# Performance work log

Measured on AMD Instinct MI355X. Metric: run time of the kernel, lower is better.

## Reference

```python
import jax, jax.numpy as jnp
import numpy as np

N_NODES = 50000
N_EDGES = 500000
H_DIM = 128
BN_EPS = 1e-5


def setup_inputs() -> dict:
    key = jax.random.key(0)
    k1, k2, k3, k4 = jax.random.split(key, 4)
    ent_emb = jax.random.normal(k1, (N_NODES, H_DIM), dtype=jnp.float32)
    neigh_w = jax.random.normal(k2, (H_DIM, H_DIM), dtype=jnp.float32) * 0.05
    gamma = jnp.ones((H_DIM,), dtype=jnp.float32)
    beta = jnp.zeros((H_DIM,), dtype=jnp.float32)
    src = jax.random.randint(k3, (N_EDGES,), 0, N_NODES, dtype=jnp.int32)
    dst = jax.random.randint(k4, (N_EDGES,), 0, N_NODES, dtype=jnp.int32)
    return {"ent_emb": ent_emb, "neigh_w": neigh_w, "gamma": gamma,
            "beta": beta, "src": src, "dst": dst}


def reference(ent_emb, neigh_w, gamma, beta, src, dst):
    # u_dot_v: per-edge dot product of src and dst node embeddings -> [E]
    e_src = ent_emb[src]                      # [E, D] gather
    scores = jnp.sum(e_src * ent_emb[dst], axis=-1)  # [E]

    # edge_softmax: softmax over incoming edges of each destination node
    seg_max = jax.ops.segment_max(scores, dst, num_segments=N_NODES)
    seg_max = jnp.where(jnp.isfinite(seg_max), seg_max, 0.0)  # empty nodes
    ex = jnp.exp(scores - seg_max[dst])
    denom = jax.ops.segment_sum(ex, dst, num_segments=N_NODES)
    norm = ex / denom[dst]                    # [E]

    # u_mul_e + sum: weighted scatter-sum of src embeddings into dst nodes
    neigh = jax.ops.segment_sum(e_src * norm[:, None], dst,
                                num_segments=N_NODES)  # [N, D]

    # linear + BatchNorm1d (training mode, batch stats) + tanh
    h = neigh @ neigh_w
    mu = jnp.mean(h, axis=0)
    var = jnp.var(h, axis=0)                  # biased, matches torch BN
    h = (h - mu) * jax.lax.rsqrt(var + BN_EPS) * gamma + beta
    return jnp.tanh(h)
```

## Files before the change

kernel.cpp:

```cpp
#include <hip/hip_runtime.h>
#include <hip/hip_bf16.h>
#include <math.h>

#define N_NODES 50000
#define N_EDGES 500000
#define H_DIM   128
#define BN_EPS  1e-5f
#define GEMM_GRID ((N_NODES + 31) / 32)
#define SCAN_NBLK ((N_NODES + 255) / 256)
#define RED_NBLK  64

typedef __attribute__((ext_vector_type(8))) short short8;
typedef __attribute__((ext_vector_type(4))) float floatx4;

__device__ __forceinline__ ushort f2bf(float x)
{
    unsigned u = __float_as_uint(x);
    unsigned r = (u + 0x7FFFu + ((u >> 16) & 1u)) >> 16;
    return (ushort)r;
}

__global__ __launch_bounds__(256) void cvt_w_kernel(
    const float* __restrict__ W, ushort* __restrict__ wt)
{
    int i = blockIdx.x * 256 + threadIdx.x;
    if (i >= H_DIM * H_DIM) return;
    int k = i >> 7, c = i & 127;
    wt[c * 128 + k] = f2bf(W[i]);
}

__global__ __launch_bounds__(256) void hist_kernel(
    const int* __restrict__ dst, int* __restrict__ deg)
{
    int e = blockIdx.x * blockDim.x + threadIdx.x;
    if (e < N_EDGES) atomicAdd(&deg[dst[e]], 1);
}

__global__ __launch_bounds__(256) void scan_partial_kernel(
    const int* __restrict__ deg, int* __restrict__ blocksum)
{
    __shared__ int red[256];
    int t = threadIdx.x;
    int i = blockIdx.x * 256 + t;
    red[t] = (i < N_NODES) ? deg[i] : 0;
    __syncthreads();
    #pragma unroll
    for (int off = 128; off; off >>= 1) {
        if (t < off) red[t] += red[t + off];
        __syncthreads();
    }
    if (t == 0) blocksum[blockIdx.x] = red[0];
}

__global__ __launch_bounds__(256) void scan_final_kernel(
    const int* __restrict__ deg, const int* __restrict__ blocksum,
    int* __restrict__ rowptr, int* __restrict__ cursor)
{
    __shared__ int bs[256];
    __shared__ int s[256];
    int t = threadIdx.x;

    bs[t] = (t < SCAN_NBLK) ? blocksum[t] : 0;
    __syncthreads();
    for (int off = 1; off < 256; off <<= 1) {
        int v = (t >= off) ? bs[t - off] : 0;
        __syncthreads();
        bs[t] += v;
        __syncthreads();
    }
    int blockoff = (blockIdx.x == 0) ? 0 : bs[blockIdx.x - 1];

    int i = blockIdx.x * 256 + t;
    int v = (i < N_NODES) ? deg[i] : 0;
    s[t] = v;
    __syncthreads();
    for (int off = 1; off < 256; off <<= 1) {
        int u = (t >= off) ? s[t - off] : 0;
        __syncthreads();
        s[t] += u;
        __syncthreads();
    }
    int excl = s[t] - v + blockoff;
    if (i < N_NODES) {
        rowptr[i] = excl;
        cursor[i] = excl;
        if (i == N_NODES - 1) rowptr[N_NODES] = excl + v;
    }
}

__global__ __launch_bounds__(256) void csr_scatter_kernel(
    const int* __restrict__ src, const int* __restrict__ dst,
    int* __restrict__ cursor, int* __restrict__ csr_src)
{
    int e = blockIdx.x * blockDim.x + threadIdx.x;
    if (e >= N_EDGES) return;
    int pos = atomicAdd(&cursor[dst[e]], 1);
    csr_src[pos] = src[e];
}

__global__ __launch_bounds__(256) void node_aggregate_kernel(
    const float* __restrict__ emb,
    const int* __restrict__ rowptr,
    const int* __restrict__ csr_src,
    float* __restrict__ neigh)
{
    int node = blockIdx.x * 8 + (threadIdx.x >> 5);
    int lane = threadIdx.x & 31;
    if (node >= N_NODES) return;

    int beg = rowptr[node];
    int end = rowptr[node + 1];

    const float4 b = *((const float4*)(emb + (size_t)node * H_DIM) + lane);

    float m = -INFINITY;
    float denom = 0.f;
    float4 acc = {0.f, 0.f, 0.f, 0.f};

    int e = beg;

    for (; e + 8 <= end; e += 8) {
        float4 a[8];
        float  p[8];
        #pragma unroll
        for (int u = 0; u < 8; ++u) {
            int s = csr_src[e + u];
            a[u] = *((const float4*)(emb + (size_t)s * H_DIM) + lane);
        }
        #pragma unroll
        for (int u = 0; u < 8; ++u)
            p[u] = a[u].x * b.x + a[u].y * b.y + a[u].z * b.z + a[u].w * b.w;
        #pragma unroll
        for (int off = 16; off; off >>= 1) {
            #pragma unroll
            for (int u = 0; u < 8; ++u)
                p[u] += __shfl_xor(p[u], off);
        }
        float mn = m;
        #pragma unroll
        for (int u = 0; u < 8; ++u) mn = fmaxf(mn, p[u]);
        float corr = __expf(m - mn);
        float w[8];
        #pragma unroll
        for (int u = 0; u < 8; ++u) w[u] = __expf(p[u] - mn);
        float ws = 0.f;
        #pragma unroll
        for (int u = 0; u < 8; ++u) ws += w[u];
        denom = denom * corr + ws;
        float sx = 0.f, sy = 0.f, sz = 0.f, sw = 0.f;
        #pragma unroll
        for (int u = 0; u < 8; ++u) {
            sx += a[u].x * w[u];
            sy += a[u].y * w[u];
            sz += a[u].z * w[u];
            sw += a[u].w * w[u];
        }
        acc.x = acc.x * corr + sx;
        acc.y = acc.y * corr + sy;
        acc.z = acc.z * corr + sz;
        acc.w = acc.w * corr + sw;
        m = mn;
    }

    if (e + 4 <= end) {
        float4 a[4];
        float  p[4];
        #pragma unroll
        for (int u = 0; u < 4; ++u) {
            int s = csr_src[e + u];
            a[u] = *((const float4*)(emb + (size_t)s * H_DIM) + lane);
        }
        #pragma unroll
        for (int u = 0; u < 4; ++u)
            p[u] = a[u].x * b.x + a[u].y * b.y + a[u].z * b.z + a[u].w * b.w;
        #pragma unroll
        for (int off = 16; off; off >>= 1) {
            #pragma unroll
            for (int u = 0; u < 4; ++u)
                p[u] += __shfl_xor(p[u], off);
        }
        float mn = fmaxf(fmaxf(fmaxf(p[0], p[1]), fmaxf(p[2], p[3])), m);
        float corr = __expf(m - mn);
        float w[4];
        #pragma unroll
        for (int u = 0; u < 4; ++u) w[u] = __expf(p[u] - mn);
        denom = denom * corr + w[0] + w[1] + w[2] + w[3];
        acc.x = acc.x * corr + a[0].x*w[0] + a[1].x*w[1] + a[2].x*w[2] + a[3].x*w[3];
        acc.y = acc.y * corr + a[0].y*w[0] + a[1].y*w[1] + a[2].y*w[2] + a[3].y*w[3];
        acc.z = acc.z * corr + a[0].z*w[0] + a[1].z*w[1] + a[2].z*w[2] + a[3].z*w[3];
        acc.w = acc.w * corr + a[0].w*w[0] + a[1].w*w[1] + a[2].w*w[2] + a[3].w*w[3];
        m = mn;
        e += 4;
    }

    for (; e < end; ++e) {
        int s = csr_src[e];
        float4 a = *((const float4*)(emb + (size_t)s * H_DIM) + lane);
        float p = a.x * b.x + a.y * b.y + a.z * b.z + a.w * b.w;
        #pragma unroll
        for (int off = 16; off; off >>= 1)
            p += __shfl_xor(p, off);
        float mn   = fmaxf(m, p);
        float corr = __expf(m - mn);
        float w    = __expf(p - mn);
        denom = denom * corr + w;
        acc.x = acc.x * corr + a.x * w;
        acc.y = acc.y * corr + a.y * w;
        acc.z = acc.z * corr + a.z * w;
        acc.w = acc.w * corr + a.w * w;
        m = mn;
    }

    float inv = (end > beg) ? (1.0f / denom) : 0.f;
    float4 o = {acc.x * inv, acc.y * inv, acc.z * inv, acc.w * inv};
    *((float4*)(neigh + (size_t)node * H_DIM) + lane) = o;
}

__global__ __launch_bounds__(256) void gemm_stats_kernel(
    const float* __restrict__ neigh,
    const ushort* __restrict__ wt,
    float* __restrict__ h,
    float* __restrict__ partial)
{
    __shared__ ushort A_s[32 * 128];
    __shared__ ushort W_s[128 * 128];
    __shared__ float  red_s[128 * 9];
    __shared__ float  red_q[128 * 9];

    int t  = threadIdx.x;
    int r0 = blockIdx.x * 32;

    for (int g = t; g < 32 * 16; g += 256) {
        int r = g >> 4, gc = g & 15;
        int gr = r0 + r;
        float4 x0 = {0.f,0.f,0.f,0.f}, x1 = {0.f,0.f,0.f,0.f};
        if (gr < N_NODES) {
            const float4* p = (const float4*)(neigh + (size_t)gr * H_DIM + gc * 8);
            x0 = p[0]; x1 = p[1];
        }
        ushort v[8] = {f2bf(x0.x), f2bf(x0.y), f2bf(x0.z), f2bf(x0.w),
                       f2bf(x1.x), f2bf(x1.y), f2bf(x1.z), f2bf(x1.w)};
        int idx = r * 128 + ((gc * 8) ^ ((r & 7) << 3));
        *(short8*)&A_s[idx] = *(short8*)v;
    }
    for (int g = t; g < 128 * 16; g += 256) {
        int c = g >> 4, gk = g & 15;
        short8 v = *(const short8*)(wt + (size_t)c * 128 + gk * 8);
        int idx = c * 128 + ((gk * 8) ^ ((c & 7) << 3));
        *(short8*)&W_s[idx] = v;
    }
    __syncthreads();

    int w    = t >> 6;
    int lane = t & 63;
    int rbase = (w >> 1) * 16;
    int c0    = (w & 1) * 64;
    int l15   = lane & 15;
    int kgrp  = lane >> 4;
    int arow  = rbase + l15;
    int k0l   = kgrp * 8;

    floatx4 acc[4] = {{0.f,0.f,0.f,0.f},{0.f,0.f,0.f,0.f},
                      {0.f,0.f,0.f,0.f},{0.f,0.f,0.f,0.f}};

    #pragma unroll
    for (int ks = 0; ks < 4; ++ks) {
        int k0 = ks * 32 + k0l;
        short8 af = *(const short8*)&A_s[arow * 128 + (k0 ^ ((arow & 7) << 3))];
        #pragma unroll
        for (int ct = 0; ct < 4; ++ct) {
            int col = c0 + ct * 16 + l15;
            short8 bf = *(const short8*)&W_s[col * 128 + (k0 ^ ((col & 7) << 3))];
            acc[ct] = __builtin_amdgcn_mfma_f32_16x16x32_bf16(af, bf, acc[ct], 0, 0, 0);
        }
    }

    int contrib = (w >> 1) * 4 + kgrp;
    #pragma unroll
    for (int ct = 0; ct < 4; ++ct) {
        int col = c0 + ct * 16 + l15;
        float ps = 0.f, pq = 0.f;
        #pragma unroll
        for (int reg = 0; reg < 4; ++reg) {
            float v = acc[ct][reg];
            int gr = r0 + rbase + kgrp * 4 + reg;
            if (gr < N_NODES) h[(size_t)gr * H_DIM + col] = v;
            ps += v;
            pq += v * v;
        }
        red_s[col * 9 + contrib] = ps;
        red_q[col * 9 + contrib] = pq;
    }
    __syncthreads();

    float s = 0.f;
    if (t < 128) {
        #pragma unroll
        for (int q = 0; q < 8; ++q) s += red_s[t * 9 + q];
    } else {
        #pragma unroll
        for (int q = 0; q < 8; ++q) s += red_q[(t - 128) * 9 + q];
    }
    partial[(size_t)blockIdx.x * 256 + t] = s;
}

__global__ __launch_bounds__(256) void reduce_partials_kernel(
    const float* __restrict__ partial, float* __restrict__ partial2)
{
    int t = threadIdx.x;
    int g = blockIdx.x;
    float s = 0.f;
    for (int b = g; b < GEMM_GRID; b += RED_NBLK)
        s += partial[(size_t)b * 256 + t];
    partial2[(size_t)g * 256 + t] = s;
}

__global__ __launch_bounds__(1024) void bn_stats_kernel(
    const float* __restrict__ partial2,
    const float* __restrict__ gamma,
    const float* __restrict__ beta,
    float* __restrict__ scale,
    float* __restrict__ shift)
{
    __shared__ float tot[4][256];
    __shared__ float tot2[256];
    int v = threadIdx.x & 255;
    int q = threadIdx.x >> 8;
    float s = 0.f;
    for (int b = q; b < RED_NBLK; b += 4)
        s += partial2[(size_t)b * 256 + v];
    tot[q][v] = s;
    __syncthreads();
    if (threadIdx.x < 256)
        tot2[v] = tot[0][v] + tot[1][v] + tot[2][v] + tot[3][v];
    __syncthreads();
    if (threadIdx.x < 128) {
        int c = threadIdx.x;
        float cs = tot2[c];
        float cq = tot2[c + 128];
        const float invN = 1.0f / (float)N_NODES;
        float mu  = cs * invN;
        float var = cq * invN - mu * mu;
        float sc  = gamma[c] * rsqrtf(var + BN_EPS);
        scale[c] = sc;
        shift[c] = beta[c] - mu * sc;
    }
}

__global__ __launch_bounds__(256) void bn_tanh_kernel(
    float* __restrict__ h,
    const float* __restrict__ scale,
    const float* __restrict__ shift)
{
    size_t i = (size_t)blockIdx.x * blockDim.x + threadIdx.x;
    size_t idx4 = i * 4;
    if (idx4 >= (size_t)N_NODES * H_DIM) return;
    int c = (int)(idx4 & (H_DIM - 1));
    float4 v = *(float4*)(h + idx4);
    v.x = tanhf(v.x * scale[c + 0] + shift[c + 0]);
    v.y = tanhf(v.y * scale[c + 1] + shift[c + 1]);
    v.z = tanhf(v.z * scale[c + 2] + shift[c + 2]);
    v.w = tanhf(v.w * scale[c + 3] + shift[c + 3]);
    *(float4*)(h + idx4) = v;
}

extern "C" void kernel_launch(void* const* d_in, const int* in_sizes, int n_in,
                              void* d_out, int out_size, void* d_ws, size_t ws_size,
                              hipStream_t stream)
{
    const float* ent_emb = (const float*)d_in[0];
    const float* neigh_w = (const float*)d_in[1];
    const float* gamma   = (const float*)d_in[2];
    const float* beta    = (const float*)d_in[3];
    const int*   src     = (const int*)d_in[4];
    const int*   dst     = (const int*)d_in[5];
    float* out = (float*)d_out;

    float*  neigh    = (float*)d_ws;
    int*    deg      = (int*)(neigh + (size_t)N_NODES * H_DIM);
    int*    rowptr   = deg + N_NODES;
    int*    cursor   = rowptr + N_NODES + 1;
    int*    csr_src  = cursor + N_NODES;
    int*    blocksum = csr_src + N_EDGES;
    float*  partial  = (float*)(blocksum + SCAN_NBLK);
    float*  partial2 = partial + (size_t)GEMM_GRID * 256;
    ushort* wt       = (ushort*)(partial2 + (size_t)RED_NBLK * 256);
    float*  scale    = (float*)(wt + H_DIM * H_DIM);
    float*  shift    = scale + H_DIM;

    hipMemsetAsync(deg, 0, N_NODES * sizeof(int), stream);

    cvt_w_kernel<<<(H_DIM * H_DIM + 255) / 256, 256, 0, stream>>>(neigh_w, wt);

    hist_kernel<<<(N_EDGES + 255) / 256, 256, 0, stream>>>(dst, deg);
    scan_partial_kernel<<<SCAN_NBLK, 256, 0, stream>>>(deg, blocksum);
    scan_final_kernel<<<SCAN_NBLK, 256, 0, stream>>>(deg, blocksum, rowptr, cursor);
    csr_scatter_kernel<<<(N_EDGES + 255) / 256, 256, 0, stream>>>(src, dst, cursor, csr_src);

    node_aggregate_kernel<<<(N_NODES + 7) / 8, 256, 0, stream>>>(
        ent_emb, rowptr, csr_src, neigh);

    gemm_stats_kernel<<<GEMM_GRID, 256, 0, stream>>>(neigh, wt, out, partial);
    reduce_partials_kernel<<<RED_NBLK, 256, 0, stream>>>(partial, partial2);
    bn_stats_kernel<<<1, 1024, 0, stream>>>(partial2, gamma, beta, scale, shift);
    {
        size_t total4 = (size_t)N_NODES * H_DIM / 4;
        int blocks = (int)((total4 + 255) / 256);
        bn_tanh_kernel<<<blocks, 256, 0, stream>>>(out, scale, shift);
    }
}
```

Baseline: 156.4 us.

## Fuse neighbor aggregation into GEMM kernel and merge weight convert into histogram

The edge-softmax aggregation now runs inside the GEMM+stats kernel, writing each node's aggregated row as bf16 straight into the swizzled shared-memory A tile. This removes the fp32 neigh intermediate (a write and re-read of about 25 MB) and one launch. The weight transpose/convert is folded into the histogram kernel to drop another launch. In exchange each block does 4 aggregation rows per 32-thread group sequentially, and the block holds ~40KB+ of LDS during the gather phase, so occupancy and latency hiding during the gather may drop (launch_bounds 256,3).

```diff
diff --git a/kernel.cpp b/kernel.cpp
--- a/kernel.cpp
+++ b/kernel.cpp
@@ -20,20 +20,16 @@
     return (ushort)r;
 }
 
-__global__ __launch_bounds__(256) void cvt_w_kernel(
+__global__ __launch_bounds__(256) void hist_cvt_kernel(
+    const int* __restrict__ dst, int* __restrict__ deg,
     const float* __restrict__ W, ushort* __restrict__ wt)
-{
-    int i = blockIdx.x * 256 + threadIdx.x;
-    if (i >= H_DIM * H_DIM) return;
-    int k = i >> 7, c = i & 127;
-    wt[c * 128 + k] = f2bf(W[i]);
-}
-
-__global__ __launch_bounds__(256) void hist_kernel(
-    const int* __restrict__ dst, int* __restrict__ deg)
 {
     int e = blockIdx.x * blockDim.x + threadIdx.x;
     if (e < N_EDGES) atomicAdd(&deg[dst[e]], 1);
+    if (e < H_DIM * H_DIM) {
+        int k = e >> 7, c = e & 127;
+        wt[c * 128 + k] = f2bf(W[e]);
+    }
 }
 
 __global__ __launch_bounds__(256) void scan_partial_kernel(
@@ -98,126 +94,10 @@
     csr_src[pos] = src[e];
 }
 
-__global__ __launch_bounds__(256) void node_aggregate_kernel(
+__global__ __launch_bounds__(256, 3) void fused_agg_gemm_kernel(
     const float* __restrict__ emb,
     const int* __restrict__ rowptr,
     const int* __restrict__ csr_src,
-    float* __restrict__ neigh)
-{
-    int node = blockIdx.x * 8 + (threadIdx.x >> 5);
-    int lane = threadIdx.x & 31;
-    if (node >= N_NODES) return;
-
-    int beg = rowptr[node];
-    int end = rowptr[node + 1];
-
-    const float4 b = *((const float4*)(emb + (size_t)node * H_DIM) + lane);
-
-    float m = -INFINITY;
-    float denom = 0.f;
-    float4 acc = {0.f, 0.f, 0.f, 0.f};
-
-    int e = beg;
-
-    for (; e + 8 <= end; e += 8) {
-        float4 a[8];
-        float  p[8];
-        #pragma unroll
-        for (int u = 0; u < 8; ++u) {
-            int s = csr_src[e + u];
-            a[u] = *((const float4*)(emb + (size_t)s * H_DIM) + lane);
-        }
-        #pragma unroll
-        for (int u = 0; u < 8; ++u)
-            p[u] = a[u].x * b.x + a[u].y * b.y + a[u].z * b.z + a[u].w * b.w;
-        #pragma unroll
-        for (int off = 16; off; off >>= 1) {
-            #pragma unroll
-            for (int u = 0; u < 8; ++u)
-                p[u] += __shfl_xor(p[u], off);
-        }
-        float mn = m;
-        #pragma unroll
-        for (int u = 0; u < 8; ++u) mn = fmaxf(mn, p[u]);
-        float corr = __expf(m - mn);
-        float w[8];
-        #pragma unroll
-        for (int u = 0; u < 8; ++u) w[u] = __expf(p[u] - mn);
-        float ws = 0.f;
-        #pragma unroll
-        for (int u = 0; u < 8; ++u) ws += w[u];
-        denom = denom * corr + ws;
-        float sx = 0.f, sy = 0.f, sz = 0.f, sw = 0.f;
-        #pragma unroll
-        for (int u = 0; u < 8; ++u) {
-            sx += a[u].x * w[u];
-            sy += a[u].y * w[u];
-            sz += a[u].z * w[u];
-            sw += a[u].w * w[u];
-        }
-        acc.x = acc.x * corr + sx;
-        acc.y = acc.y * corr + sy;
-        acc.z = acc.z * corr + sz;
-        acc.w = acc.w * corr + sw;
-        m = mn;
-    }
-
-    if (e + 4 <= end) {
-        float4 a[4];
-        float  p[4];
-        #pragma unroll
-        for (int u = 0; u < 4; ++u) {
-            int s = csr_src[e + u];
-            a[u] = *((const float4*)(emb + (size_t)s * H_DIM) + lane);
-        }
-        #pragma unroll
-        for (int u = 0; u < 4; ++u)
-            p[u] = a[u].x * b.x + a[u].y * b.y + a[u].z * b.z + a[u].w * b.w;
-        #pragma unroll
-        for (int off = 16; off; off >>= 1) {
-            #pragma unroll
-            for (int u = 0; u < 4; ++u)
-                p[u] += __shfl_xor(p[u], off);
-        }
-        float mn = fmaxf(fmaxf(fmaxf(p[0], p[1]), fmaxf(p[2], p[3])), m);
-        float corr = __expf(m - mn);
-        float w[4];
-        #pragma unroll
-        for (int u = 0; u < 4; ++u) w[u] = __expf(p[u] - mn);
-        denom = denom * corr + w[0] + w[1] + w[2] + w[3];
-        acc.x = acc.x * corr + a[0].x*w[0] + a[1].x*w[1] + a[2].x*w[2] + a[3].x*w[3];
-        acc.y = acc.y * corr + a[0].y*w[0] + a[1].y*w[1] + a[2].y*w[2] + a[3].y*w[3];
-        acc.z = acc.z * corr + a[0].z*w[0] + a[1].z*w[1] + a[2].z*w[2] + a[3].z*w[3];
-        acc.w = acc.w * corr + a[0].w*w[0] + a[1].w*w[1] + a[2].w*w[2] + a[3].w*w[3];
-        m = mn;
-        e += 4;
-    }
-
-    for (; e < end; ++e) {
-        int s = csr_src[e];
-        float4 a = *((const float4*)(emb + (size_t)s * H_DIM) + lane);
-        float p = a.x * b.x + a.y * b.y + a.z * b.z + a.w * b.w;
-        #pragma unroll
-        for (int off = 16; off; off >>= 1)
-            p += __shfl_xor(p, off);
-        float mn   = fmaxf(m, p);
-        float corr = __expf(m - mn);
-        float w    = __expf(p - mn);
-        denom = denom * corr + w;
-        acc.x = acc.x * corr + a.x * w;
-        acc.y = acc.y * corr + a.y * w;
-        acc.z = acc.z * corr + a.z * w;
-        acc.w = acc.w * corr + a.w * w;
-        m = mn;
-    }
-
-    float inv = (end > beg) ? (1.0f / denom) : 0.f;
-    float4 o = {acc.x * inv, acc.y * inv, acc.z * inv, acc.w * inv};
-    *((float4*)(neigh + (size_t)node * H_DIM) + lane) = o;
-}
-
-__global__ __launch_bounds__(256) void gemm_stats_kernel(
-    const float* __restrict__ neigh,
     const ushort* __restrict__ wt,
     float* __restrict__ h,
     float* __restrict__ partial)
@@ -230,38 +110,145 @@
     int t  = threadIdx.x;
     int r0 = blockIdx.x * 32;
 
-    for (int g = t; g < 32 * 16; g += 256) {
-        int r = g >> 4, gc = g & 15;
-        int gr = r0 + r;
-        float4 x0 = {0.f,0.f,0.f,0.f}, x1 = {0.f,0.f,0.f,0.f};
-        if (gr < N_NODES) {
-            const float4* p = (const float4*)(neigh + (size_t)gr * H_DIM + gc * 8);
-            x0 = p[0]; x1 = p[1];
-        }
-        ushort v[8] = {f2bf(x0.x), f2bf(x0.y), f2bf(x0.z), f2bf(x0.w),
-                       f2bf(x1.x), f2bf(x1.y), f2bf(x1.z), f2bf(x1.w)};
-        int idx = r * 128 + ((gc * 8) ^ ((r & 7) << 3));
-        *(short8*)&A_s[idx] = *(short8*)v;
-    }
     for (int g = t; g < 128 * 16; g += 256) {
         int c = g >> 4, gk = g & 15;
         short8 v = *(const short8*)(wt + (size_t)c * 128 + gk * 8);
         int idx = c * 128 + ((gk * 8) ^ ((c & 7) << 3));
         *(short8*)&W_s[idx] = v;
     }
+
+    int grp  = t >> 5;
+    int lane = t & 31;
+
+    for (int ri = 0; ri < 4; ++ri) {
+        int row  = ri * 8 + grp;
+        int node = r0 + row;
+        float4 o = {0.f, 0.f, 0.f, 0.f};
+
+        if (node < N_NODES) {
+            int beg = rowptr[node];
+            int end = rowptr[node + 1];
+            const float4 b = *((const float4*)(emb + (size_t)node * H_DIM) + lane);
+
+            float m = -INFINITY;
+            float denom = 0.f;
+            float4 acc = {0.f, 0.f, 0.f, 0.f};
+
+            int e = beg;
+            for (; e + 8 <= end; e += 8) {
+                float4 a[8];
+                float  p[8];
+                #pragma unroll
+                for (int u = 0; u < 8; ++u) {
+                    int s = csr_src[e + u];
+                    a[u] = *((const float4*)(emb + (size_t)s * H_DIM) + lane);
+                }
+                #pragma unroll
+                for (int u = 0; u < 8; ++u)
+                    p[u] = a[u].x * b.x + a[u].y * b.y + a[u].z * b.z + a[u].w * b.w;
+                #pragma unroll
+                for (int off = 16; off; off >>= 1) {
+                    #pragma unroll
+                    for (int u = 0; u < 8; ++u)
+                        p[u] += __shfl_xor(p[u], off);
+                }
+                float mn = m;
+                #pragma unroll
+                for (int u = 0; u < 8; ++u) mn = fmaxf(mn, p[u]);
+                float corr = __expf(m - mn);
+                float w[8];
+                #pragma unroll
+                for (int u = 0; u < 8; ++u) w[u] = __expf(p[u] - mn);
+                float wsum = 0.f;
+                #pragma unroll
+                for (int u = 0; u < 8; ++u) wsum += w[u];
+                denom = denom * corr + wsum;
+                float sx = 0.f, sy = 0.f, sz = 0.f, sw = 0.f;
+                #pragma unroll
+                for (int u = 0; u < 8; ++u) {
+                    sx += a[u].x * w[u];
+                    sy += a[u].y * w[u];
+                    sz += a[u].z * w[u];
+                    sw += a[u].w * w[u];
+                }
+                acc.x = acc.x * corr + sx;
+                acc.y = acc.y * corr + sy;
+                acc.z = acc.z * corr + sz;
+                acc.w = acc.w * corr + sw;
+                m = mn;
+            }
+            if (e + 4 <= end) {
+                float4 a[4];
+                float  p[4];
+                #pragma unroll
+                for (int u = 0; u < 4; ++u) {
+                    int s = csr_src[e + u];
+                    a[u] = *((const float4*)(emb + (size_t)s * H_DIM) + lane);
+                }
+                #pragma unroll
+                for (int u = 0; u < 4; ++u)
+                    p[u] = a[u].x * b.x + a[u].y * b.y + a[u].z * b.z + a[u].w * b.w;
+                #pragma unroll
+                for (int off = 16; off; off >>= 1) {
+                    #pragma unroll
+                    for (int u = 0; u < 4; ++u)
+                        p[u] += __shfl_xor(p[u], off);
+                }
+                float mn = fmaxf(fmaxf(fmaxf(p[0], p[1]), fmaxf(p[2], p[3])), m);
+                float corr = __expf(m - mn);
+                float w[4];
+                #pragma unroll
+                for (int u = 0; u < 4; ++u) w[u] = __expf(p[u] - mn);
+                denom = denom * corr + w[0] + w[1] + w[2] + w[3];
+                acc.x = acc.x * corr + a[0].x*w[0] + a[1].x*w[1] + a[2].x*w[2] + a[3].x*w[3];
+                acc.y = acc.y * corr + a[0].y*w[0] + a[1].y*w[1] + a[2].y*w[2] + a[3].y*w[3];
+                acc.z = acc.z * corr + a[0].z*w[0] + a[1].z*w[1] + a[2].z*w[2] + a[3].z*w[3];
+                acc.w = acc.w * corr + a[0].w*w[0] + a[1].w*w[1] + a[2].w*w[2] + a[3].w*w[3];
+                m = mn;
+                e += 4;
+            }
+            for (; e < end; ++e) {
+                int s = csr_src[e];
+                float4 a = *((const float4*)(emb + (size_t)s * H_DIM) + lane);
+                float p = a.x * b.x + a.y * b.y + a.z * b.z + a.w * b.w;
+                #pragma unroll
+                for (int off = 16; off; off >>= 1)
+                    p += __shfl_xor(p, off);
+                float mn   = fmaxf(m, p);
+                float corr = __expf(m - mn);
+                float w    = __expf(p - mn);
+                denom = denom * corr + w;
+                acc.x = acc.x * corr + a.x * w;
+                acc.y = acc.y * corr + a.y * w;
+                acc.z = acc.z * corr + a.z * w;
+                acc.w = acc.w * corr + a.w * w;
+                m = mn;
+            }
+
+            float inv = (end > beg) ? (1.0f / denom) : 0.f;
+            o.x = acc.x * inv; o.y = acc.y * inv;
+            o.z = acc.z * inv; o.w = acc.w * inv;
+        }
+
+        unsigned lo = (unsigned)f2bf(o.x) | ((unsigned)f2bf(o.y) << 16);
+        unsigned hi = (unsigned)f2bf(o.z) | ((unsigned)f2bf(o.w) << 16);
+        int col = (lane * 4) ^ ((row & 7) << 3);
+        uint2 pk; pk.x = lo; pk.y = hi;
+        *(uint2*)&A_s[row * 128 + col] = pk;
+    }
     __syncthreads();
 
     int w    = t >> 6;
-    int lane = t & 63;
+    int lane64 = t & 63;
     int rbase = (w >> 1) * 16;
     int c0    = (w & 1) * 64;
-    int l15   = lane & 15;
-    int kgrp  = lane >> 4;
+    int l15   = lane64 & 15;
+    int kgrp  = lane64 >> 4;
     int arow  = rbase + l15;
     int k0l   = kgrp * 8;
 
-    floatx4 acc[4] = {{0.f,0.f,0.f,0.f},{0.f,0.f,0.f,0.f},
-                      {0.f,0.f,0.f,0.f},{0.f,0.f,0.f,0.f}};
+    floatx4 acc4[4] = {{0.f,0.f,0.f,0.f},{0.f,0.f,0.f,0.f},
+                       {0.f,0.f,0.f,0.f},{0.f,0.f,0.f,0.f}};
 
     #pragma unroll
     for (int ks = 0; ks < 4; ++ks) {
@@ -271,7 +258,7 @@
         for (int ct = 0; ct < 4; ++ct) {
             int col = c0 + ct * 16 + l15;
             short8 bf = *(const short8*)&W_s[col * 128 + (k0 ^ ((col & 7) << 3))];
-            acc[ct] = __builtin_amdgcn_mfma_f32_16x16x32_bf16(af, bf, acc[ct], 0, 0, 0);
+            acc4[ct] = __builtin_amdgcn_mfma_f32_16x16x32_bf16(af, bf, acc4[ct], 0, 0, 0);
         }
     }
 
@@ -282,7 +269,7 @@
         float ps = 0.f, pq = 0.f;
         #pragma unroll
         for (int reg = 0; reg < 4; ++reg) {
-            float v = acc[ct][reg];
+            float v = acc4[ct][reg];
             int gr = r0 + rbase + kgrp * 4 + reg;
             if (gr < N_NODES) h[(size_t)gr * H_DIM + col] = v;
             ps += v;
@@ -297,7 +284,7 @@
     if (t < 128) {
         #pragma unroll
         for (int q = 0; q < 8; ++q) s += red_s[t * 9 + q];
-    } else {
+    } else if (t < 256) {
         #pragma unroll
         for (int q = 0; q < 8; ++q) s += red_q[(t - 128) * 9 + q];
     }
@@ -376,8 +363,7 @@
     const int*   dst     = (const int*)d_in[5];
     float* out = (float*)d_out;
 
-    float*  neigh    = (float*)d_ws;
-    int*    deg      = (int*)(neigh + (size_t)N_NODES * H_DIM);
+    int*    deg      = (int*)d_ws;
     int*    rowptr   = deg + N_NODES;
     int*    cursor   = rowptr + N_NODES + 1;
     int*    csr_src  = cursor + N_NODES;
@@ -390,17 +376,14 @@
 
     hipMemsetAsync(deg, 0, N_NODES * sizeof(int), stream);
 
-    cvt_w_kernel<<<(H_DIM * H_DIM + 255) / 256, 256, 0, stream>>>(neigh_w, wt);
-
-    hist_kernel<<<(N_EDGES + 255) / 256, 256, 0, stream>>>(dst, deg);
+    hist_cvt_kernel<<<(N_EDGES + 255) / 256, 256, 0, stream>>>(dst, deg, neigh_w, wt);
     scan_partial_kernel<<<SCAN_NBLK, 256, 0, stream>>>(deg, blocksum);
     scan_final_kernel<<<SCAN_NBLK, 256, 0, stream>>>(deg, blocksum, rowptr, cursor);
     csr_scatter_kernel<<<(N_EDGES + 255) / 256, 256, 0, stream>>>(src, dst, cursor, csr_src);
 
-    node_aggregate_kernel<<<(N_NODES + 7) / 8, 256, 0, stream>>>(
-        ent_emb, rowptr, csr_src, neigh);
-
-    gemm_stats_kernel<<<GEMM_GRID, 256, 0, stream>>>(neigh, wt, out, partial);
+    fused_agg_gemm_kernel<<<GEMM_GRID, 256, 0, stream>>>(
+        ent_emb, rowptr, csr_src, wt, out, partial);
+
     reduce_partials_kernel<<<RED_NBLK, 256, 0, stream>>>(partial, partial2);
     bn_stats_kernel<<<1, 1024, 0, stream>>>(partial2, gamma, beta, scale, shift);
     {
```

After: 164.6 us. +5.2%, slower.
